# Kernel tuning notes

Measured on AMD Instinct MI355X. Metric: run time of the kernel, lower is better.

Reference implementation:

```python
import jax, jax.numpy as jnp
import numpy as np

# Grid config: output_shape = [2, 40, 400, 352, 16] -> sparse_shape = [41, 400, 352]
B, Dz, Hy, Wx = 2, 41, 400, 352
N_PER = 20000          # active voxels per sample
C_IN = 128
# Strided SparseConv3d(k=3, s=2, p=1) output spatial dims
Do, Ho, Wo = (Dz + 2 - 3) // 2 + 1, (Hy + 2 - 3) // 2 + 1, (Wx + 2 - 3) // 2 + 1


def setup_inputs() -> dict:
    rng = np.random.default_rng(0)
    coors_list = []
    for b in range(B):
        # unique voxel positions per sample (z limited to original 40-deep grid)
        flat = rng.choice((Dz - 1) * Hy * Wx, size=N_PER, replace=False)
        z = flat // (Hy * Wx)
        r = flat % (Hy * Wx)
        y = r // Wx
        x = r % Wx
        coors_list.append(np.stack([np.full(N_PER, b), z, y, x], axis=1))
    coors = jnp.asarray(np.concatenate(coors_list, 0), jnp.int32)  # [N,4]

    key = jax.random.key(0)
    k1, k2, k3, k4 = jax.random.split(key, 4)
    N = B * N_PER
    voxel_features = jax.random.normal(k1, (N, C_IN), jnp.float32)
    W1 = jax.random.normal(k2, (3, 3, 3, C_IN, 16), jnp.float32) * (1.0 / np.sqrt(27 * C_IN))
    W2 = jax.random.normal(k3, (3, 3, 3, 16, 16), jnp.float32) * (1.0 / np.sqrt(27 * 16))
    W3 = jax.random.normal(k4, (3, 3, 3, 16, 32), jnp.float32) * (1.0 / np.sqrt(27 * 16))
    return dict(voxel_features=voxel_features, coors=coors, W1=W1, W2=W2, W3=W3, batch_size=B)


def _offsets():
    o = jnp.stack(jnp.meshgrid(jnp.arange(3), jnp.arange(3), jnp.arange(3), indexing='ij'), -1)
    return o.reshape(27, 3)  # [27,3] kernel taps


def reference(voxel_features, coors, W1, W2, W3, batch_size):
    N = voxel_features.shape[0]
    offs = _offsets()

    # --- rulebook: dense index grid, padded by 1 so neighbor lookups never go OOB
    grid = jnp.full((batch_size, Dz + 2, Hy + 2, Wx + 2), -1, jnp.int32)
    grid = grid.at[coors[:, 0], coors[:, 1] + 1, coors[:, 2] + 1, coors[:, 3] + 1].set(
        jnp.arange(N, dtype=jnp.int32))
    # neighbor voxel index for every active site and every 3x3x3 tap: [N,27]
    nbr = grid[coors[:, 0:1], coors[:, 1:2] + offs[:, 0], coors[:, 2:3] + offs[:, 1],
               coors[:, 3:4] + offs[:, 2]]
    valid = (nbr >= 0)[..., None]
    nbr_c = jnp.clip(nbr, 0, N - 1)

    def subm(feat, W):  # submanifold conv: gather -> GEMM, output only on active sites
        Cin, Cout = W.shape[3], W.shape[4]
        g = jnp.where(valid, feat[nbr_c], 0.0)                      # [N,27,Cin]
        return jnp.einsum('nkc,kcd->nd', g, W.reshape(27, Cin, Cout))

    x = jax.nn.relu(subm(voxel_features, W1))   # SubMConv3d(128->16) + ReLU
    x = jax.nn.relu(subm(x, W2))                # SubMConv3d(16->16, same rulebook) + ReLU

    # --- SparseConv3d(16->32, k=3, stride=2, pad=1): scatter-add into downsampled grid
    contrib = jnp.einsum('nc,kcd->nkd', x, W3.reshape(27, 16, 32))  # [N,27,32]
    oz = coors[:, 1:2] + 1 - offs[:, 0]  # p_in + pad - k, must be even and in range
    oy = coors[:, 2:3] + 1 - offs[:, 1]
    ox = coors[:, 3:4] + 1 - offs[:, 2]
    pz, py, px = oz // 2, oy // 2, ox // 2
    ok = ((oz % 2 == 0) & (oy % 2 == 0) & (ox % 2 == 0) &
          (pz >= 0) & (pz < Do) & (py >= 0) & (py < Ho) & (px >= 0) & (px < Wo))
    total = batch_size * Do * Ho * Wo
    flat = coors[:, 0:1] * (Do * Ho * Wo) + pz * (Ho * Wo) + py * Wo + px
    flat = jnp.where(ok, flat, total)  # invalid -> dummy slot
    out = jnp.zeros((total + 1, 32), x.dtype).at[flat.reshape(-1)].add(
        contrib.reshape(-1, 32))[:total]
    out = jax.nn.relu(out).reshape(batch_size, Do, Ho, Wo, 32)  # dense() of sparse output
    return out
```

## Files before the change

kernel.cpp:

```cpp
#include <hip/hip_runtime.h>

#define B_   2
#define DZ   41
#define HY   400
#define WX   352
#define NVOX 40000
#define PD   43
#define PH   402
#define PW   354
#define DO_  21
#define HO_  200
#define WO_  176
#define C1   128
#define GRID_CELLS (B_*PD*PH*PW)
#define OUT_POS    (B_*DO_*HO_*WO_)


__global__ void k_build(const int* __restrict__ coors, unsigned short* __restrict__ grid) {
    int n = blockIdx.x * blockDim.x + threadIdx.x;
    if (n >= NVOX) return;
    int b = coors[4*n+0], z = coors[4*n+1], y = coors[4*n+2], x = coors[4*n+3];
    grid[((b*PD + z+1)*PH + y+1)*PW + x+1] = (unsigned short)(n + 1);
}

__global__ void k_nbr(const int* __restrict__ coors, const unsigned short* __restrict__ grid,
                      int* __restrict__ nbr) {
    int i = blockIdx.x * blockDim.x + threadIdx.x;
    if (i >= NVOX * 27) return;
    int n = i / 27, k = i % 27;
    int b = coors[4*n+0], z = coors[4*n+1], y = coors[4*n+2], x = coors[4*n+3];
    int dz = k / 9, dy = (k / 3) % 3, dx = k % 3;
    nbr[i] = (int)grid[((b*PD + z+dz)*PH + y+dy)*PW + x+dx] - 1;
}

__global__ void k_subm1(const float* __restrict__ feat,
                        const float* __restrict__ W1,
                        const int* __restrict__ nbr, float* __restrict__ x1) {
    __shared__ int s_nbr[16][27];
    int base = blockIdx.x * 16;
    for (int i = threadIdx.x; i < 16*27; i += 256) {
        int v = i / 27, k = i % 27;
        int n = base + v;
        s_nbr[v][k] = (n < NVOX) ? nbr[n*27 + k] : -1;
    }
    __syncthreads();
    int v = threadIdx.x >> 4, d = threadIdx.x & 15;
    int n = base + v;
    if (n >= NVOX) return;
    float acc = 0.f;
    for (int k = 0; k < 27; ++k) {
        int idx = s_nbr[v][k];
        if (idx < 0) continue;
        const float* f = feat + (size_t)idx * C1;
        const float* w = W1 + k * C1 * 16 + d;
        #pragma unroll 8
        for (int c = 0; c < C1; ++c)
            acc += f[c] * w[c * 16];
    }
    x1[n*16 + d] = fmaxf(acc, 0.f);
}

__global__ void k_subm2(const float* __restrict__ x1,
                        const float* __restrict__ W2,
                        const int* __restrict__ nbr, float* __restrict__ x2) {
    __shared__ int   s_nbr[16][27];
    __shared__ float s_w2[27*16*16];
    for (int i = threadIdx.x; i < 27*16*16; i += 256) s_w2[i] = W2[i];
    int base = blockIdx.x * 16;
    for (int i = threadIdx.x; i < 16*27; i += 256) {
        int v = i / 27, k = i % 27;
        int n = base + v;
        s_nbr[v][k] = (n < NVOX) ? nbr[n*27 + k] : -1;
    }
    __syncthreads();
    int v = threadIdx.x >> 4, d = threadIdx.x & 15;
    int n = base + v;
    if (n >= NVOX) return;
    float acc = 0.f;
    for (int k = 0; k < 27; ++k) {
        int idx = s_nbr[v][k];
        if (idx < 0) continue;
        const float* xp = x1 + idx * 16;
        const float* w  = s_w2 + k * 256 + d;
        #pragma unroll
        for (int c = 0; c < 16; ++c) acc += xp[c] * w[c * 16];
    }
    x2[n*16 + d] = fmaxf(acc, 0.f);
}

__device__ __forceinline__ int axis_taps(int pcoord, int outdim, int* ds, int* ps) {
    if (pcoord & 1) { ds[0] = 1; ps[0] = pcoord >> 1; return 1; }
    int h = pcoord >> 1, nu = 0;
    if (h < outdim) { ds[nu] = 0; ps[nu] = h; nu++; }
    ds[nu] = 2; ps[nu] = h - 1; nu++;
    return nu;
}

__global__ void k_scatter(const float* __restrict__ x2,
                          const float* __restrict__ W3,
                          const int* __restrict__ coors,
                          float* __restrict__ out) {
    int v = threadIdx.x >> 5, d = threadIdx.x & 31;
    int n = blockIdx.x * 8 + v;
    if (n >= NVOX) return;
    int b  = coors[4*n+0];
    int zp = coors[4*n+1] + 1, yp = coors[4*n+2] + 1, xp = coors[4*n+3] + 1;
    int dz[2], pz[2], dy[2], py[2], dx[2], px[2];
    int nz = axis_taps(zp, DO_, dz, pz);
    int ny = axis_taps(yp, HO_, dy, py);
    int nx = axis_taps(xp, WO_, dx, px);
    const float4* xr = (const float4*)(x2 + (size_t)n * 16);
    float r[16];
    *(float4*)(r + 0)  = xr[0];
    *(float4*)(r + 4)  = xr[1];
    *(float4*)(r + 8)  = xr[2];
    *(float4*)(r + 12) = xr[3];
    int bofs = b * (DO_*HO_*WO_);
    for (int iz = 0; iz < nz; ++iz)
        for (int iy = 0; iy < ny; ++iy)
            for (int ix = 0; ix < nx; ++ix) {
                int k = dz[iz]*9 + dy[iy]*3 + dx[ix];
                int p = bofs + (pz[iz]*HO_ + py[iy])*WO_ + px[ix];
                const float* w = W3 + k*512 + d;
                float acc = 0.f;
                #pragma unroll
                for (int c = 0; c < 16; ++c) acc += r[c] * w[c * 32];
                atomicAdd(out + (size_t)p * 32 + d, acc);
            }
}

__global__ void k_relu(const int* __restrict__ coors, float* __restrict__ out) {
    int v = threadIdx.x >> 5, d = threadIdx.x & 31;
    int n = blockIdx.x * 8 + v;
    if (n >= NVOX) return;
    int b  = coors[4*n+0];
    int zp = coors[4*n+1] + 1, yp = coors[4*n+2] + 1, xp = coors[4*n+3] + 1;
    int dz[2], pz[2], dy[2], py[2], dx[2], px[2];
    int nz = axis_taps(zp, DO_, dz, pz);
    int ny = axis_taps(yp, HO_, dy, py);
    int nx = axis_taps(xp, WO_, dx, px);
    int bofs = b * (DO_*HO_*WO_);
    for (int iz = 0; iz < nz; ++iz)
        for (int iy = 0; iy < ny; ++iy)
            for (int ix = 0; ix < nx; ++ix) {
                int p = bofs + (pz[iz]*HO_ + py[iy])*WO_ + px[ix];
                size_t o = (size_t)p * 32 + d;
                out[o] = fmaxf(out[o], 0.f);
            }
}

extern "C" void kernel_launch(void* const* d_in, const int* in_sizes, int n_in,
                              void* d_out, int out_size, void* d_ws, size_t ws_size,
                              hipStream_t stream) {
    const float* feat  = (const float*)d_in[0];
    const int*   coors = (const int*)d_in[1];
    const float* W1    = (const float*)d_in[2];
    const float* W2    = (const float*)d_in[3];
    const float* W3    = (const float*)d_in[4];
    float* out = (float*)d_out;

    char* ws = (char*)d_ws;
    size_t off = 0;
    unsigned short* grid = (unsigned short*)(ws + off);
    off += (((size_t)GRID_CELLS*2) + 255) & ~(size_t)255;
    int* nbr  = (int*)(ws + off); off += (((size_t)NVOX*27*4)   + 255) & ~(size_t)255;
    float* x1 = (float*)(ws + off); off += (((size_t)NVOX*16*4) + 255) & ~(size_t)255;
    float* x2 = (float*)(ws + off);

    hipMemsetAsync(grid, 0x00, (size_t)GRID_CELLS * 2, stream);
    hipMemsetAsync(out, 0x00, (size_t)out_size * sizeof(float), stream);
    k_build<<<(NVOX + 255) / 256, 256, 0, stream>>>(coors, grid);
    k_nbr<<<(NVOX*27 + 255) / 256, 256, 0, stream>>>(coors, grid, nbr);
    k_subm1<<<(NVOX + 15) / 16, 256, 0, stream>>>(feat, W1, nbr, x1);
    k_subm2<<<(NVOX + 15) / 16, 256, 0, stream>>>(x1, W2, nbr, x2);
    k_scatter<<<(NVOX + 7) / 8, 256, 0, stream>>>(x2, W3, coors, out);
    k_relu<<<(NVOX + 7) / 8, 256, 0, stream>>>(coors, out);
}
```

Before: 304.5 us.

## Compact neighbor lists, vectorize feature loads, replace memsets with zero kernels

Builds a compacted per-voxel list of valid (tap, index) pairs so the submanifold convs loop only over existing neighbors instead of all 27 taps with branches. It also vectorizes feature reads with float4, drops the shared-memory W2 staging in subm2, and replaces hipMemsetAsync with custom float4 zero kernels. With a sparse grid most taps are empty, so divergence and wasted iterations drop. In exchange the neighbor-build kernel becomes serial per thread, with 27 grid probes and scattered writes.

```diff
diff --git a/kernel.cpp b/kernel.cpp
--- a/kernel.cpp
+++ b/kernel.cpp
@@ -13,8 +13,15 @@
 #define WO_  176
 #define C1   128
 #define GRID_CELLS (B_*PD*PH*PW)
-#define OUT_POS    (B_*DO_*HO_*WO_)
+#define OUT_ELEMS  (B_*DO_*HO_*WO_*32)
+#define OUT_F4     (OUT_ELEMS/4)
+#define GRID_F4    (GRID_CELLS*2/16)
 
+
+__global__ void k_zero4(float4* __restrict__ p, int n4) {
+    int i = blockIdx.x * 256 + threadIdx.x;
+    if (i < n4) p[i] = make_float4(0.f, 0.f, 0.f, 0.f);
+}
 
 __global__ void k_build(const int* __restrict__ coors, unsigned short* __restrict__ grid) {
     int n = blockIdx.x * blockDim.x + threadIdx.x;
@@ -23,67 +30,80 @@
     grid[((b*PD + z+1)*PH + y+1)*PW + x+1] = (unsigned short)(n + 1);
 }
 
-__global__ void k_nbr(const int* __restrict__ coors, const unsigned short* __restrict__ grid,
-                      int* __restrict__ nbr) {
-    int i = blockIdx.x * blockDim.x + threadIdx.x;
-    if (i >= NVOX * 27) return;
-    int n = i / 27, k = i % 27;
+__global__ void k_nbrc(const int* __restrict__ coors, const unsigned short* __restrict__ grid,
+                       int* __restrict__ nbrc) {
+    int n = blockIdx.x * 256 + threadIdx.x;
+    if (n >= NVOX) return;
     int b = coors[4*n+0], z = coors[4*n+1], y = coors[4*n+2], x = coors[4*n+3];
-    int dz = k / 9, dy = (k / 3) % 3, dx = k % 3;
-    nbr[i] = (int)grid[((b*PD + z+dz)*PH + y+dy)*PW + x+dx] - 1;
+    int* dst = nbrc + n * 28;
+    int cnt = 0;
+    for (int k = 0; k < 27; ++k) {
+        int dz = k / 9, dy = (k / 3) % 3, dx = k % 3;
+        int id = (int)grid[((b*PD + z+dz)*PH + y+dy)*PW + x+dx] - 1;
+        if (id >= 0) dst[1 + cnt++] = (k << 16) | id;
+    }
+    dst[0] = cnt;
 }
 
 __global__ void k_subm1(const float* __restrict__ feat,
                         const float* __restrict__ W1,
-                        const int* __restrict__ nbr, float* __restrict__ x1) {
-    __shared__ int s_nbr[16][27];
+                        const int* __restrict__ nbrc, float* __restrict__ x1) {
+    __shared__ int s_p[16][28];
     int base = blockIdx.x * 16;
-    for (int i = threadIdx.x; i < 16*27; i += 256) {
-        int v = i / 27, k = i % 27;
+    for (int i = threadIdx.x; i < 16*28; i += 256) {
+        int v = i / 28, j = i % 28;
         int n = base + v;
-        s_nbr[v][k] = (n < NVOX) ? nbr[n*27 + k] : -1;
+        s_p[v][j] = (n < NVOX) ? nbrc[n*28 + j] : 0;
     }
     __syncthreads();
     int v = threadIdx.x >> 4, d = threadIdx.x & 15;
     int n = base + v;
     if (n >= NVOX) return;
+    int cnt = s_p[v][0];
     float acc = 0.f;
-    for (int k = 0; k < 27; ++k) {
-        int idx = s_nbr[v][k];
-        if (idx < 0) continue;
-        const float* f = feat + (size_t)idx * C1;
-        const float* w = W1 + k * C1 * 16 + d;
+    for (int t = 1; t <= cnt; ++t) {
+        int pk = s_p[v][t];
+        int k = pk >> 16, idx = pk & 0xFFFF;
+        const float4* f4 = (const float4*)(feat + (size_t)idx * C1);
+        const float* w = W1 + k * (C1*16) + d;
         #pragma unroll 8
-        for (int c = 0; c < C1; ++c)
-            acc += f[c] * w[c * 16];
+        for (int c4 = 0; c4 < 32; ++c4) {
+            float4 f = f4[c4];
+            acc += f.x * w[(c4*4+0)*16];
+            acc += f.y * w[(c4*4+1)*16];
+            acc += f.z * w[(c4*4+2)*16];
+            acc += f.w * w[(c4*4+3)*16];
+        }
     }
     x1[n*16 + d] = fmaxf(acc, 0.f);
 }
 
 __global__ void k_subm2(const float* __restrict__ x1,
                         const float* __restrict__ W2,
-                        const int* __restrict__ nbr, float* __restrict__ x2) {
-    __shared__ int   s_nbr[16][27];
-    __shared__ float s_w2[27*16*16];
-    for (int i = threadIdx.x; i < 27*16*16; i += 256) s_w2[i] = W2[i];
+                        const int* __restrict__ nbrc, float* __restrict__ x2) {
+    __shared__ int s_p[16][28];
     int base = blockIdx.x * 16;
-    for (int i = threadIdx.x; i < 16*27; i += 256) {
-        int v = i / 27, k = i % 27;
+    for (int i = threadIdx.x; i < 16*28; i += 256) {
+        int v = i / 28, j = i % 28;
         int n = base + v;
-        s_nbr[v][k] = (n < NVOX) ? nbr[n*27 + k] : -1;
+        s_p[v][j] = (n < NVOX) ? nbrc[n*28 + j] : 0;
     }
     __syncthreads();
     int v = threadIdx.x >> 4, d = threadIdx.x & 15;
     int n = base + v;
     if (n >= NVOX) return;
+    int cnt = s_p[v][0];
     float acc = 0.f;
-    for (int k = 0; k < 27; ++k) {
-        int idx = s_nbr[v][k];
-        if (idx < 0) continue;
-        const float* xp = x1 + idx * 16;
-        const float* w  = s_w2 + k * 256 + d;
-        #pragma unroll
-        for (int c = 0; c < 16; ++c) acc += xp[c] * w[c * 16];
+    for (int t = 1; t <= cnt; ++t) {
+        int pk = s_p[v][t];
+        int k = pk >> 16, idx = pk & 0xFFFF;
+        const float4* xr = (const float4*)(x1 + (size_t)idx * 16);
+        float4 a0 = xr[0], a1 = xr[1], a2 = xr[2], a3 = xr[3];
+        const float* w = W2 + k * 256 + d;
+        acc += a0.x*w[0*16]  + a0.y*w[1*16]  + a0.z*w[2*16]  + a0.w*w[3*16]
+             + a1.x*w[4*16]  + a1.y*w[5*16]  + a1.z*w[6*16]  + a1.w*w[7*16]
+             + a2.x*w[8*16]  + a2.y*w[9*16]  + a2.z*w[10*16] + a2.w*w[11*16]
+             + a3.x*w[12*16] + a3.y*w[13*16] + a3.z*w[14*16] + a3.w*w[15*16];
     }
     x2[n*16 + d] = fmaxf(acc, 0.f);
 }
@@ -163,16 +183,16 @@
     size_t off = 0;
     unsigned short* grid = (unsigned short*)(ws + off);
     off += (((size_t)GRID_CELLS*2) + 255) & ~(size_t)255;
-    int* nbr  = (int*)(ws + off); off += (((size_t)NVOX*27*4)   + 255) & ~(size_t)255;
+    int* nbrc = (int*)(ws + off); off += (((size_t)NVOX*28*4)  + 255) & ~(size_t)255;
     float* x1 = (float*)(ws + off); off += (((size_t)NVOX*16*4) + 255) & ~(size_t)255;
     float* x2 = (float*)(ws + off);
 
-    hipMemsetAsync(grid, 0x00, (size_t)GRID_CELLS * 2, stream);
-    hipMemsetAsync(out, 0x00, (size_t)out_size * sizeof(float), stream);
+    k_zero4<<<(OUT_F4  + 255) / 256, 256, 0, stream>>>((float4*)out,  OUT_F4);
+    k_zero4<<<(GRID_F4 + 255) / 256, 256, 0, stream>>>((float4*)grid, GRID_F4);
     k_build<<<(NVOX + 255) / 256, 256, 0, stream>>>(coors, grid);
-    k_nbr<<<(NVOX*27 + 255) / 256, 256, 0, stream>>>(coors, grid, nbr);
-    k_subm1<<<(NVOX + 15) / 16, 256, 0, stream>>>(feat, W1, nbr, x1);
-    k_subm2<<<(NVOX + 15) / 16, 256, 0, stream>>>(x1, W2, nbr, x2);
+    k_nbrc<<<(NVOX + 255) / 256, 256, 0, stream>>>(coors, grid, nbrc);
+    k_subm1<<<(NVOX + 15) / 16, 256, 0, stream>>>(feat, W1, nbrc, x1);
+    k_subm2<<<(NVOX + 15) / 16, 256, 0, stream>>>(x1, W2, nbrc, x2);
     k_scatter<<<(NVOX + 7) / 8, 256, 0, stream>>>(x2, W3, coors, out);
     k_relu<<<(NVOX + 7) / 8, 256, 0, stream>>>(coors, out);
 }
```

Result: slower. 338.3 us (+11.1%).
